# Kernel tuning notes

Measured on AMD Instinct MI355X. Metric: run time of the kernel, lower is better.

Reference implementation:

```python
import jax, jax.numpy as jnp
import numpy as np

C = 512
M = 8            # n_heads
G = 32           # GroupNorm groups
EPS = 1e-6


def setup_inputs() -> dict:
    key = jax.random.key(0)
    ks = jax.random.split(key, 7)
    x = jax.random.normal(ks[0], (2, C, 64, 64), dtype=jnp.float32)
    gn_weight = jnp.ones((C,), jnp.float32)
    gn_bias = jnp.zeros((C,), jnp.float32)
    qkv_w = jax.random.normal(ks[1], (3 * C, C), jnp.float32) * (1.0 / np.sqrt(C))
    qkv_b = jnp.zeros((3 * C,), jnp.float32)
    # source zero-inits proj_out; we use small random weights so the attention
    proj_w = jax.random.normal(ks[2], (C, C), jnp.float32) * (0.02 / np.sqrt(C))
    proj_b = jnp.zeros((C,), jnp.float32)
    return {"x": x, "gn_weight": gn_weight, "gn_bias": gn_bias,
            "qkv_w": qkv_w, "qkv_b": qkv_b, "proj_w": proj_w, "proj_b": proj_b}


def _forward(x, gn_weight, gn_bias, qkv_w, qkv_b, proj_w, proj_b):
    b, c, H, W = x.shape
    n = H * W
    d = c // M
    xf = x.reshape(b, c, n)

    # GroupNorm(32, c, eps=1e-6, affine)
    xg = xf.reshape(b, G, (c // G) * n)
    mu = xg.mean(axis=-1, keepdims=True)
    var = xg.var(axis=-1, keepdims=True)
    xn = ((xg - mu) * jax.lax.rsqrt(var + EPS)).reshape(b, c, n)
    xn = xn * gn_weight[None, :, None] + gn_bias[None, :, None]

    # 1x1 conv -> qkv, then legacy reshape-then-split
    qkv = jnp.einsum('oc,bcn->bon', qkv_w, xn) + qkv_b[None, :, None]  # (b, 3c, n)
    qkv = qkv.reshape(b * M, 3 * d, n)
    q, k, v = qkv[:, :d], qkv[:, d:2 * d], qkv[:, 2 * d:]

    scale = 1.0 / np.sqrt(np.sqrt(d))
    w = jnp.einsum('Bdi,Bdj->Bij', q * scale, k * scale)  # (b*m, n, n)
    w = jax.nn.softmax(w, axis=-1)
    a = jnp.einsum('Bin,Bdn->Bdi', w, v)                  # (b*m, d, n)
    a = a.reshape(b, c, n)

    h = jnp.einsum('oc,bcn->bon', proj_w, a) + proj_b[None, :, None]
    # NOTE: source reassigns x = norm(x) before the residual add.
    return (xn + h).reshape(b, c, H, W)


def reference(x, gn_weight, gn_bias, qkv_w, qkv_b, proj_w, proj_b):
    return _forward(x, gn_weight, gn_bias, qkv_w, qkv_b, proj_w, proj_b)
```

## Files before the change

kernel.cpp:

```cpp
#include <hip/hip_runtime.h>
#include <cstdint>
#include <cstddef>

typedef __attribute__((ext_vector_type(8))) short short8;
typedef __attribute__((ext_vector_type(4))) float f32x4;

#define QSCALE 0.18033688011112043f

__device__ __forceinline__ float bf2f(unsigned short u) {
  return __uint_as_float(((unsigned)u) << 16);
}
__device__ __forceinline__ unsigned short f2bf(float f) {
  unsigned u = __float_as_uint(f);
  u += 0x7fffu + ((u >> 16) & 1u);
  return (unsigned short)(u >> 16);
}
__device__ __forceinline__ unsigned packbf2(float a, float b) {
  unsigned ua = __float_as_uint(a) + 0x8000u;
  unsigned ub = __float_as_uint(b) + 0x8000u;
  return __builtin_amdgcn_perm(ub, ua, 0x07060302u);
}
__device__ __forceinline__ unsigned cvtpk(float a, float b) {
  unsigned r;
  asm("v_cvt_pk_bf16_f32 %0, %1, %2" : "=v"(r) : "v"(a), "v"(b));
  return r;
}
__device__ __forceinline__ short8 mk8(unsigned a, unsigned b, unsigned c, unsigned d) {
  union { unsigned u[4]; short8 s; } x;
  x.u[0] = a; x.u[1] = b; x.u[2] = c; x.u[3] = d;
  return x.s;
}
__device__ __forceinline__ void g2l16(const void* g, void* l) {
  __builtin_amdgcn_global_load_lds(
      (const __attribute__((address_space(1))) unsigned int*)g,
      (__attribute__((address_space(3))) unsigned int*)l, 16, 0, 0);
}

__global__ __launch_bounds__(256) void k_wconv(const float* __restrict__ wqf,
                                               const float* __restrict__ wpf,
                                               unsigned short* __restrict__ wq,
                                               unsigned short* __restrict__ wp) {
  int i = blockIdx.x * 256 + threadIdx.x;
  if (i < 196608) {
    float4 v = ((const float4*)wqf)[i];
    ushort4 u;
    u.x = f2bf(v.x); u.y = f2bf(v.y); u.z = f2bf(v.z); u.w = f2bf(v.w);
    ((ushort4*)wq)[i] = u;
  } else {
    int k = i - 196608;
    float4 v = ((const float4*)wpf)[k];
    ushort4 u;
    u.x = f2bf(v.x); u.y = f2bf(v.y); u.z = f2bf(v.z); u.w = f2bf(v.w);
    ((ushort4*)wp)[k] = u;
  }
}

__global__ __launch_bounds__(256) void k_gnpart(const float* __restrict__ x,
                                                float* __restrict__ part) {
  int blk = blockIdx.x;
  int bg = blk >> 4, slice = blk & 15;
  const float4* base = (const float4*)(x + (size_t)bg * 65536 + (size_t)slice * 4096);
  int t = threadIdx.x;
  float s = 0.f, q = 0.f;
#pragma unroll
  for (int i = 0; i < 4; ++i) {
    float4 v = base[t + i * 256];
    s += v.x + v.y + v.z + v.w;
    q += v.x * v.x + v.y * v.y + v.z * v.z + v.w * v.w;
  }
#pragma unroll
  for (int off = 1; off < 64; off <<= 1) {
    s += __shfl_xor(s, off);
    q += __shfl_xor(q, off);
  }
  __shared__ float red[8];
  int wid = t >> 6;
  if ((t & 63) == 0) { red[wid * 2] = s; red[wid * 2 + 1] = q; }
  __syncthreads();
  if (t == 0) {
    float S = red[0] + red[2] + red[4] + red[6];
    float Q = red[1] + red[3] + red[5] + red[7];
    part[blk * 2] = S;
    part[blk * 2 + 1] = Q;
  }
}

__global__ void k_gnfin(const float* __restrict__ part, float* __restrict__ stats) {
  int t = threadIdx.x;
  float S = 0.f, Q = 0.f;
#pragma unroll
  for (int i = 0; i < 16; ++i) {
    S += part[(t * 16 + i) * 2];
    Q += part[(t * 16 + i) * 2 + 1];
  }
  float mean = S * (1.f / 65536.f);
  float var = Q * (1.f / 65536.f) - mean * mean;
  stats[t * 2] = mean;
  stats[t * 2 + 1] = rsqrtf(var + 1e-6f);
}

__global__ __launch_bounds__(256) void k_gnnorm(const float* __restrict__ x,
                                                const float* __restrict__ gnw,
                                                const float* __restrict__ gnb,
                                                const float* __restrict__ stats,
                                                unsigned short* __restrict__ xn,
                                                unsigned short* __restrict__ xnT) {
  __shared__ float T[64 * 65];
  const int t = threadIdx.x;
  const int n0 = blockIdx.x * 64, c0 = blockIdx.y * 64, bb = blockIdx.z;
#pragma unroll
  for (int p = 0; p < 4; ++p) {
    int s = p * 256 + t;
    int row = s >> 4, seg = s & 15;
    int c = c0 + row;
    int gi = bb * 32 + (c >> 4);
    float mean = stats[gi * 2], rstd = stats[gi * 2 + 1];
    float gw = gnw[c] * rstd;
    float gb = gnb[c] - mean * gw;
    float4 v = *(const float4*)(x + ((size_t)bb * 512 + c) * 4096 + n0 + seg * 4);
    float f0 = v.x * gw + gb, f1 = v.y * gw + gb, f2 = v.z * gw + gb, f3 = v.w * gw + gb;
    ushort4 u;
    u.x = f2bf(f0); u.y = f2bf(f1); u.z = f2bf(f2); u.w = f2bf(f3);
    *(ushort4*)(xn + ((size_t)bb * 512 + c) * 4096 + n0 + seg * 4) = u;
    T[(seg * 4 + 0) * 65 + row] = f0;
    T[(seg * 4 + 1) * 65 + row] = f1;
    T[(seg * 4 + 2) * 65 + row] = f2;
    T[(seg * 4 + 3) * 65 + row] = f3;
  }
  __syncthreads();
#pragma unroll
  for (int p = 0; p < 4; ++p) {
    int s = p * 256 + t;
    int nl = s >> 4, cs = s & 15;
    float f0 = T[nl * 65 + cs * 4 + 0];
    float f1 = T[nl * 65 + cs * 4 + 1];
    float f2 = T[nl * 65 + cs * 4 + 2];
    float f3 = T[nl * 65 + cs * 4 + 3];
    ushort4 u;
    u.x = f2bf(f0); u.y = f2bf(f1); u.z = f2bf(f2); u.w = f2bf(f3);
    *(ushort4*)(xnT + ((size_t)bb * 4096 + n0 + nl) * 512 + c0 + cs * 4) = u;
  }
}

template <int MODE>
__global__ __launch_bounds__(256) void k_gemm(
    const unsigned short* __restrict__ A,
    const unsigned short* __restrict__ Bt,
    const float* __restrict__ bias,
    unsigned short* __restrict__ outA,
    unsigned short* __restrict__ outT,
    const unsigned short* __restrict__ resid,
    float* __restrict__ outF,
    int Mo) {
  __shared__ char lds[34816];
  const int t = threadIdx.x;
  const int lane = t & 63;
  const int g = lane >> 4, ln = lane & 15;
  const int wid = t >> 6, wr = wid >> 1, wc = wid & 1;
  const int bn0 = blockIdx.x * 128, bm0 = blockIdx.y * 128, bb = blockIdx.z;

  const unsigned short* Ab = A + (size_t)bm0 * 512;
  const unsigned short* Bb = Bt + ((size_t)bb * 4096 + bn0) * 512;

  f32x4 acc[4][4];
#pragma unroll
  for (int m = 0; m < 4; ++m)
#pragma unroll
    for (int n = 0; n < 4; ++n) acc[m][n] = f32x4{0.f, 0.f, 0.f, 0.f};

#pragma unroll 1
  for (int kt = 0; kt < 8; ++kt) {
#pragma unroll
    for (int p = 0; p < 4; ++p) {
      int s = p * 256 + t;
      int row = s >> 3;
      int csg = (s & 7) ^ (row & 7);
      g2l16(Ab + (size_t)row * 512 + kt * 64 + csg * 8,
            &lds[(p * 256 + (t & ~63)) * 16]);
    }
#pragma unroll
    for (int p = 0; p < 4; ++p) {
      int s = p * 256 + t;
      int row = s >> 3;
      int csg = (s & 7) ^ (row & 7);
      g2l16(Bb + (size_t)row * 512 + kt * 64 + csg * 8,
            &lds[16384 + (p * 256 + (t & ~63)) * 16]);
    }
    __syncthreads();
#pragma unroll
    for (int kk = 0; kk < 2; ++kk) {
      short8 af[4], bfr[4];
#pragma unroll
      for (int m = 0; m < 4; ++m) {
        int row = wr * 64 + m * 16 + ln;
        int cs = (kk * 4 + g) ^ (row & 7);
        af[m] = *(const short8*)&lds[row * 128 + cs * 16];
      }
#pragma unroll
      for (int n = 0; n < 4; ++n) {
        int row = wc * 64 + n * 16 + ln;
        int cs = (kk * 4 + g) ^ (row & 7);
        bfr[n] = *(const short8*)&lds[16384 + row * 128 + cs * 16];
      }
      __builtin_amdgcn_s_setprio(1);
#pragma unroll
      for (int m = 0; m < 4; ++m)
#pragma unroll
        for (int n = 0; n < 4; ++n)
          acc[m][n] = __builtin_amdgcn_mfma_f32_16x16x32_bf16(af[m], bfr[n], acc[m][n], 0, 0, 0);
      __builtin_amdgcn_s_setprio(0);
    }
    __syncthreads();
  }

  if (MODE == 0) {
#pragma unroll
    for (int m = 0; m < 4; ++m)
#pragma unroll
      for (int n = 0; n < 4; ++n)
#pragma unroll
        for (int r = 0; r < 4; ++r) {
          int ol = wr * 64 + m * 16 + g * 4 + r;
          int jl = wc * 64 + n * 16 + ln;
          int o = bm0 + ol, j = bn0 + jl;
          float v = acc[m][n][r] + bias[o];
          unsigned short bv = f2bf(v);
          if ((o % 192) >= 128) {
            int jp = (j & ~63) | (j & 32) | ((j & 0xC) << 1) | ((j & 16) >> 2) | (j & 3);
            outA[((size_t)bb * 1536 + o) * 4096 + jp] = bv;
          }
          *(unsigned short*)&lds[jl * 272 + ol * 2] = bv;
        }
    __syncthreads();
#pragma unroll
    for (int p = 0; p < 8; ++p) {
      int s = p * 256 + t;
      int jl = s >> 4, cs = s & 15;
      int oo = bm0 + cs * 8;
      if ((oo % 192) < 128) {
        short8 v = *(const short8*)&lds[jl * 272 + cs * 16];
        *(short8*)&outT[((size_t)bb * 4096 + bn0 + jl) * 1536 + oo] = v;
      }
    }
  } else {
#pragma unroll
    for (int m = 0; m < 4; ++m)
#pragma unroll
      for (int n = 0; n < 4; ++n)
#pragma unroll
        for (int r = 0; r < 4; ++r) {
          int o = bm0 + wr * 64 + m * 16 + g * 4 + r;
          int j = bn0 + wc * 64 + n * 16 + ln;
          size_t idx = ((size_t)bb * 512 + o) * 4096 + j;
          outF[idx] = acc[m][n][r] + bias[o] + bf2f(resid[idx]);
        }
  }
}

__global__ __launch_bounds__(256, 2) void k_attn(const unsigned short* __restrict__ qkv,
                                                 const unsigned short* __restrict__ qkvT,
                                                 unsigned short* __restrict__ aT) {
  __shared__ char lds[49152];
  const int t = threadIdx.x, lane = t & 63;
  const int g = lane >> 4, ln = lane & 15;
  const int wid = t >> 6;
  const int h = blockIdx.y, bb = blockIdx.z;
  const int q0 = blockIdx.x * 128 + wid * 32;

  int kaddr[2][4], vaddr[2][4];
#pragma unroll
  for (int kk = 0; kk < 2; ++kk)
#pragma unroll
    for (int f = 0; f < 4; ++f) {
      int row = f * 16 + ln;
      int off = row * 128 + (((kk * 4 + g) ^ (row & 7)) << 4);
      kaddr[kk][f] = off;
      vaddr[kk][f] = 24576 + off;
    }

  const unsigned short* kS[2];
  const unsigned short* vS[2];
  int ldst[2];
#pragma unroll
  for (int p = 0; p < 2; ++p) {
    int s = p * 256 + t;
    int row = s >> 3, csg = (s & 7) ^ (row & 7);
    kS[p] = qkvT + ((size_t)bb * 4096 + row) * 1536 + 192 * h + 64 + csg * 8;
    vS[p] = qkv + ((size_t)bb * 1536 + 192 * h + 128 + row) * 4096 + csg * 8;
    ldst[p] = (p * 256 + (t & ~63)) * 16;
  }

  short8 qf[2][2];
#pragma unroll
  for (int qt = 0; qt < 2; ++qt)
#pragma unroll
    for (int kk = 0; kk < 2; ++kk) {
      short8 v = *(const short8*)(qkvT + ((size_t)bb * 4096 + q0 + qt * 16 + ln) * 1536 +
                                  192 * h + kk * 32 + g * 8);
#pragma unroll
      for (int e = 0; e < 8; ++e) {
        float f = bf2f((unsigned short)v[e]) * QSCALE;
        v[e] = (short)f2bf(f);
      }
      qf[qt][kk] = v;
    }

  const short8 onesb = mk8(0x3F803F80u, 0x3F803F80u, 0x3F803F80u, 0x3F803F80u);

  f32x4 acc[2][4];
  f32x4 lacc[2];
#pragma unroll
  for (int qt = 0; qt < 2; ++qt) {
#pragma unroll
    for (int df = 0; df < 4; ++df) acc[qt][df] = f32x4{0.f, 0.f, 0.f, 0.f};
    lacc[qt] = f32x4{0.f, 0.f, 0.f, 0.f};
  }

#pragma unroll
  for (int jt = 0; jt < 2; ++jt) {
#pragma unroll
    for (int p = 0; p < 2; ++p) {
      g2l16(kS[p], &lds[jt * 8192 + ldst[p]]);
      g2l16(vS[p], &lds[24576 + jt * 8192 + ldst[p]]);
      kS[p] += 64 * 1536;
      vS[p] += 64;
    }
  }

#pragma unroll 3
  for (int jt = 0; jt < 64; ++jt) {
    const int cur = jt % 3;
    const char* Kc = &lds[cur * 8192];
    const char* Vc = &lds[cur * 8192];
    if (jt < 63) {
      asm volatile("s_waitcnt vmcnt(4)" ::: "memory");
    } else {
      asm volatile("s_waitcnt vmcnt(0)" ::: "memory");
    }
    __builtin_amdgcn_s_barrier();
    __builtin_amdgcn_sched_barrier(0);

    if (jt < 62) {
      int nb = (jt + 2) % 3;
#pragma unroll
      for (int p = 0; p < 2; ++p) {
        g2l16(kS[p], &lds[nb * 8192 + ldst[p]]);
        g2l16(vS[p], &lds[24576 + nb * 8192 + ldst[p]]);
        kS[p] += 64 * 1536;
        vS[p] += 64;
      }
    }

    short8 kf[2][4], vf[2][4];
#pragma unroll
    for (int kk = 0; kk < 2; ++kk)
#pragma unroll
      for (int f = 0; f < 4; ++f) {
        kf[kk][f] = *(const short8*)(Kc + kaddr[kk][f]);
        vf[kk][f] = *(const short8*)(Vc + vaddr[kk][f]);
      }

#pragma unroll
    for (int qt = 0; qt < 2; ++qt) {
      f32x4 w[4];
      const f32x4 zf = f32x4{0.f, 0.f, 0.f, 0.f};
      __builtin_amdgcn_s_setprio(1);
#pragma unroll
      for (int jf = 0; jf < 4; ++jf)
        w[jf] = __builtin_amdgcn_mfma_f32_16x16x32_bf16(kf[0][jf], qf[qt][0], zf, 0, 0, 0);
#pragma unroll
      for (int jf = 0; jf < 4; ++jf)
        w[jf] = __builtin_amdgcn_mfma_f32_16x16x32_bf16(kf[1][jf], qf[qt][1], w[jf], 0, 0, 0);
      __builtin_amdgcn_s_setprio(0);

#pragma unroll
      for (int jf = 0; jf < 4; ++jf)
#pragma unroll
        for (int r = 0; r < 4; ++r)
          w[jf][r] = __builtin_amdgcn_exp2f(w[jf][r]);

      short8 pf[2];
#pragma unroll
      for (int kk = 0; kk < 2; ++kk)
        pf[kk] = mk8(cvtpk(w[2 * kk][0], w[2 * kk][1]),
                     cvtpk(w[2 * kk][2], w[2 * kk][3]),
                     cvtpk(w[2 * kk + 1][0], w[2 * kk + 1][1]),
                     cvtpk(w[2 * kk + 1][2], w[2 * kk + 1][3]));

      __builtin_amdgcn_s_setprio(1);
#pragma unroll
      for (int kk = 0; kk < 2; ++kk) {
#pragma unroll
        for (int df = 0; df < 4; ++df)
          acc[qt][df] = __builtin_amdgcn_mfma_f32_16x16x32_bf16(pf[kk], vf[kk][df], acc[qt][df], 0, 0, 0);
        lacc[qt] = __builtin_amdgcn_mfma_f32_16x16x32_bf16(pf[kk], onesb, lacc[qt], 0, 0, 0);
      }
      __builtin_amdgcn_s_setprio(0);
    }
  }

#pragma unroll
  for (int qt = 0; qt < 2; ++qt) {
#pragma unroll
    for (int r = 0; r < 4; ++r) {
      float inv = 1.f / lacc[qt][r];
      int row = q0 + qt * 16 + g * 4 + r;
#pragma unroll
      for (int df = 0; df < 4; ++df)
        aT[((size_t)bb * 4096 + row) * 512 + h * 64 + df * 16 + ln] =
            f2bf(acc[qt][df][r] * inv);
    }
  }
}

extern "C" void kernel_launch(void* const* d_in, const int* in_sizes, int n_in,
                              void* d_out, int out_size, void* d_ws, size_t ws_size,
                              hipStream_t stream) {
  const float* x     = (const float*)d_in[0];
  const float* gnw   = (const float*)d_in[1];
  const float* gnb   = (const float*)d_in[2];
  const float* qkvw  = (const float*)d_in[3];
  const float* qkvb  = (const float*)d_in[4];
  const float* projw = (const float*)d_in[5];
  const float* projb = (const float*)d_in[6];
  float* out = (float*)d_out;
  char* ws = (char*)d_ws;

  const size_t OFF_WQ   = 0;
  const size_t OFF_WP   = 1572864;
  const size_t OFF_XN   = 2097152;
  const size_t OFF_XNT  = 10485760;
  const size_t OFF_QKV  = 18874368;
  const size_t OFF_QKVT = 44040192;
  const size_t OFF_AT   = 69206016;
  const size_t OFF_PART = 77594624;
  const size_t OFF_STAT = 77602816;

  unsigned short* wq   = (unsigned short*)(ws + OFF_WQ);
  unsigned short* wp   = (unsigned short*)(ws + OFF_WP);
  unsigned short* xn   = (unsigned short*)(ws + OFF_XN);
  unsigned short* xnT  = (unsigned short*)(ws + OFF_XNT);
  unsigned short* qkv  = (unsigned short*)(ws + OFF_QKV);
  unsigned short* qkvT = (unsigned short*)(ws + OFF_QKVT);
  unsigned short* aT   = (unsigned short*)(ws + OFF_AT);
  float* part  = (float*)(ws + OFF_PART);
  float* stats = (float*)(ws + OFF_STAT);

  k_wconv<<<dim3(1024), dim3(256), 0, stream>>>(qkvw, projw, wq, wp);
  k_gnpart<<<dim3(1024), dim3(256), 0, stream>>>(x, part);
  k_gnfin<<<dim3(1), dim3(64), 0, stream>>>(part, stats);
  k_gnnorm<<<dim3(64, 8, 2), dim3(256), 0, stream>>>(x, gnw, gnb, stats, xn, xnT);
  k_gemm<0><<<dim3(32, 12, 2), dim3(256), 0, stream>>>(wq, xnT, qkvb, qkv, qkvT, nullptr, nullptr, 1536);
  k_attn<<<dim3(32, 8, 2), dim3(256), 0, stream>>>(qkv, qkvT, aT);
  k_gemm<1><<<dim3(32, 4, 2), dim3(256), 0, stream>>>(wp, aT, projb, nullptr, nullptr, xn, out, 512);
}
```

Measured before the change: 131.4 us.

## Software-pipeline attention PV with next QK/exp and merge weight-convert with GN partials

The attention loop is restructured so that the PV MFMAs for the previous key tile run interleaved, via sched_group_barrier, with the QK MFMAs and exp2 work of the current tile. V fragments and P values are carried across iterations, with a prologue and epilogue for the first and last tiles. The aim is to hide exp/convert VALU latency behind matrix work. Separately, the weight-conversion and GroupNorm partial-sum kernels are merged into a single launch to save one kernel launch. The pipelining raises register pressure, and the interleave pattern may not match the real instruction mix.

Measured after the change: 125.6 us. 1.05x faster.

```diff
diff --git a/kernel.cpp b/kernel.cpp
--- a/kernel.cpp
+++ b/kernel.cpp
@@ -15,11 +15,6 @@
   u += 0x7fffu + ((u >> 16) & 1u);
   return (unsigned short)(u >> 16);
 }
-__device__ __forceinline__ unsigned packbf2(float a, float b) {
-  unsigned ua = __float_as_uint(a) + 0x8000u;
-  unsigned ub = __float_as_uint(b) + 0x8000u;
-  return __builtin_amdgcn_perm(ub, ua, 0x07060302u);
-}
 __device__ __forceinline__ unsigned cvtpk(float a, float b) {
   unsigned r;
   asm("v_cvt_pk_bf16_f32 %0, %1, %2" : "=v"(r) : "v"(a), "v"(b));
@@ -36,52 +31,54 @@
       (__attribute__((address_space(3))) unsigned int*)l, 16, 0, 0);
 }
 
-__global__ __launch_bounds__(256) void k_wconv(const float* __restrict__ wqf,
-                                               const float* __restrict__ wpf,
-                                               unsigned short* __restrict__ wq,
-                                               unsigned short* __restrict__ wp) {
-  int i = blockIdx.x * 256 + threadIdx.x;
-  if (i < 196608) {
-    float4 v = ((const float4*)wqf)[i];
-    ushort4 u;
-    u.x = f2bf(v.x); u.y = f2bf(v.y); u.z = f2bf(v.z); u.w = f2bf(v.w);
-    ((ushort4*)wq)[i] = u;
+__global__ __launch_bounds__(256) void k_wgn(const float* __restrict__ wqf,
+                                             const float* __restrict__ wpf,
+                                             unsigned short* __restrict__ wq,
+                                             unsigned short* __restrict__ wp,
+                                             const float* __restrict__ x,
+                                             float* __restrict__ part) {
+  __shared__ float red[8];
+  const int blk = blockIdx.x;
+  const int t = threadIdx.x;
+  if (blk < 1024) {
+    int i = blk * 256 + t;
+    if (i < 196608) {
+      float4 v = ((const float4*)wqf)[i];
+      ushort4 u;
+      u.x = f2bf(v.x); u.y = f2bf(v.y); u.z = f2bf(v.z); u.w = f2bf(v.w);
+      ((ushort4*)wq)[i] = u;
+    } else {
+      int k = i - 196608;
+      float4 v = ((const float4*)wpf)[k];
+      ushort4 u;
+      u.x = f2bf(v.x); u.y = f2bf(v.y); u.z = f2bf(v.z); u.w = f2bf(v.w);
+      ((ushort4*)wp)[k] = u;
+    }
   } else {
-    int k = i - 196608;
-    float4 v = ((const float4*)wpf)[k];
-    ushort4 u;
-    u.x = f2bf(v.x); u.y = f2bf(v.y); u.z = f2bf(v.z); u.w = f2bf(v.w);
-    ((ushort4*)wp)[k] = u;
-  }
-}
-
-__global__ __launch_bounds__(256) void k_gnpart(const float* __restrict__ x,
-                                                float* __restrict__ part) {
-  int blk = blockIdx.x;
-  int bg = blk >> 4, slice = blk & 15;
-  const float4* base = (const float4*)(x + (size_t)bg * 65536 + (size_t)slice * 4096);
-  int t = threadIdx.x;
-  float s = 0.f, q = 0.f;
-#pragma unroll
-  for (int i = 0; i < 4; ++i) {
-    float4 v = base[t + i * 256];
-    s += v.x + v.y + v.z + v.w;
-    q += v.x * v.x + v.y * v.y + v.z * v.z + v.w * v.w;
-  }
-#pragma unroll
-  for (int off = 1; off < 64; off <<= 1) {
-    s += __shfl_xor(s, off);
-    q += __shfl_xor(q, off);
-  }
-  __shared__ float red[8];
-  int wid = t >> 6;
-  if ((t & 63) == 0) { red[wid * 2] = s; red[wid * 2 + 1] = q; }
-  __syncthreads();
-  if (t == 0) {
-    float S = red[0] + red[2] + red[4] + red[6];
-    float Q = red[1] + red[3] + red[5] + red[7];
-    part[blk * 2] = S;
-    part[blk * 2 + 1] = Q;
+    int b2 = blk - 1024;
+    int bg = b2 >> 4, slice = b2 & 15;
+    const float4* base = (const float4*)(x + (size_t)bg * 65536 + (size_t)slice * 4096);
+    float s = 0.f, q = 0.f;
+#pragma unroll
+    for (int i = 0; i < 4; ++i) {
+      float4 v = base[t + i * 256];
+      s += v.x + v.y + v.z + v.w;
+      q += v.x * v.x + v.y * v.y + v.z * v.z + v.w * v.w;
+    }
+#pragma unroll
+    for (int off = 1; off < 64; off <<= 1) {
+      s += __shfl_xor(s, off);
+      q += __shfl_xor(q, off);
+    }
+    int wid = t >> 6;
+    if ((t & 63) == 0) { red[wid * 2] = s; red[wid * 2 + 1] = q; }
+    __syncthreads();
+    if (t == 0) {
+      float S = red[0] + red[2] + red[4] + red[6];
+      float Q = red[1] + red[3] + red[5] + red[7];
+      part[b2 * 2] = S;
+      part[b2 * 2 + 1] = Q;
+    }
   }
 }
 
@@ -316,6 +313,9 @@
     lacc[qt] = f32x4{0.f, 0.f, 0.f, 0.f};
   }
 
+  short8 pf[2][2];
+  short8 vfp[2][4];
+
 #pragma unroll
   for (int jt = 0; jt < 2; ++jt) {
 #pragma unroll
@@ -327,15 +327,71 @@
     }
   }
 
+  {
+    asm volatile("s_waitcnt vmcnt(4)" ::: "memory");
+    __builtin_amdgcn_s_barrier();
+    __builtin_amdgcn_sched_barrier(0);
+#pragma unroll
+    for (int p = 0; p < 2; ++p) {
+      g2l16(kS[p], &lds[2 * 8192 + ldst[p]]);
+      g2l16(vS[p], &lds[24576 + 2 * 8192 + ldst[p]]);
+      kS[p] += 64 * 1536;
+      vS[p] += 64;
+    }
+    const char* Kc = &lds[0];
+    short8 kf[2][4];
+#pragma unroll
+    for (int kk = 0; kk < 2; ++kk)
+#pragma unroll
+      for (int f = 0; f < 4; ++f) kf[kk][f] = *(const short8*)(Kc + kaddr[kk][f]);
+    const f32x4 zf = f32x4{0.f, 0.f, 0.f, 0.f};
+    f32x4 w0[4], w1[4];
+    __builtin_amdgcn_s_setprio(1);
+#pragma unroll
+    for (int jf = 0; jf < 4; ++jf)
+      w0[jf] = __builtin_amdgcn_mfma_f32_16x16x32_bf16(kf[0][jf], qf[0][0], zf, 0, 0, 0);
+#pragma unroll
+    for (int jf = 0; jf < 4; ++jf)
+      w0[jf] = __builtin_amdgcn_mfma_f32_16x16x32_bf16(kf[1][jf], qf[0][1], w0[jf], 0, 0, 0);
+#pragma unroll
+    for (int jf = 0; jf < 4; ++jf)
+      w1[jf] = __builtin_amdgcn_mfma_f32_16x16x32_bf16(kf[0][jf], qf[1][0], zf, 0, 0, 0);
+#pragma unroll
+    for (int jf = 0; jf < 4; ++jf)
+      w1[jf] = __builtin_amdgcn_mfma_f32_16x16x32_bf16(kf[1][jf], qf[1][1], w1[jf], 0, 0, 0);
+    __builtin_amdgcn_s_setprio(0);
+#pragma unroll
+    for (int jf = 0; jf < 4; ++jf)
+#pragma unroll
+      for (int r = 0; r < 4; ++r) {
+        w0[jf][r] = __builtin_amdgcn_exp2f(w0[jf][r]);
+        w1[jf][r] = __builtin_amdgcn_exp2f(w1[jf][r]);
+      }
+#pragma unroll
+    for (int kk = 0; kk < 2; ++kk) {
+      pf[0][kk] = mk8(cvtpk(w0[2 * kk][0], w0[2 * kk][1]),
+                      cvtpk(w0[2 * kk][2], w0[2 * kk][3]),
+                      cvtpk(w0[2 * kk + 1][0], w0[2 * kk + 1][1]),
+                      cvtpk(w0[2 * kk + 1][2], w0[2 * kk + 1][3]));
+      pf[1][kk] = mk8(cvtpk(w1[2 * kk][0], w1[2 * kk][1]),
+                      cvtpk(w1[2 * kk][2], w1[2 * kk][3]),
+                      cvtpk(w1[2 * kk + 1][0], w1[2 * kk + 1][1]),
+                      cvtpk(w1[2 * kk + 1][2], w1[2 * kk + 1][3]));
+    }
+#pragma unroll
+    for (int kk = 0; kk < 2; ++kk)
+#pragma unroll
+      for (int f = 0; f < 4; ++f) vfp[kk][f] = *(const short8*)(Kc + vaddr[kk][f]);
+  }
+
 #pragma unroll 3
-  for (int jt = 0; jt < 64; ++jt) {
+  for (int jt = 1; jt < 64; ++jt) {
     const int cur = jt % 3;
     const char* Kc = &lds[cur * 8192];
-    const char* Vc = &lds[cur * 8192];
     if (jt < 63) {
-      asm volatile("s_waitcnt vmcnt(4)" ::: "memory");
+      asm volatile("s_waitcnt vmcnt(4) lgkmcnt(0)" ::: "memory");
     } else {
-      asm volatile("s_waitcnt vmcnt(0)" ::: "memory");
+      asm volatile("s_waitcnt vmcnt(0) lgkmcnt(0)" ::: "memory");
     }
     __builtin_amdgcn_s_barrier();
     __builtin_amdgcn_sched_barrier(0);
@@ -351,53 +407,86 @@
       }
     }
 
-    short8 kf[2][4], vf[2][4];
+    short8 kf[2][4];
 #pragma unroll
     for (int kk = 0; kk < 2; ++kk)
 #pragma unroll
-      for (int f = 0; f < 4; ++f) {
-        kf[kk][f] = *(const short8*)(Kc + kaddr[kk][f]);
-        vf[kk][f] = *(const short8*)(Vc + vaddr[kk][f]);
-      }
-
-#pragma unroll
-    for (int qt = 0; qt < 2; ++qt) {
-      f32x4 w[4];
-      const f32x4 zf = f32x4{0.f, 0.f, 0.f, 0.f};
-      __builtin_amdgcn_s_setprio(1);
-#pragma unroll
-      for (int jf = 0; jf < 4; ++jf)
-        w[jf] = __builtin_amdgcn_mfma_f32_16x16x32_bf16(kf[0][jf], qf[qt][0], zf, 0, 0, 0);
-#pragma unroll
-      for (int jf = 0; jf < 4; ++jf)
-        w[jf] = __builtin_amdgcn_mfma_f32_16x16x32_bf16(kf[1][jf], qf[qt][1], w[jf], 0, 0, 0);
-      __builtin_amdgcn_s_setprio(0);
-
-#pragma unroll
-      for (int jf = 0; jf < 4; ++jf)
-#pragma unroll
-        for (int r = 0; r < 4; ++r)
-          w[jf][r] = __builtin_amdgcn_exp2f(w[jf][r]);
-
-      short8 pf[2];
-#pragma unroll
-      for (int kk = 0; kk < 2; ++kk)
-        pf[kk] = mk8(cvtpk(w[2 * kk][0], w[2 * kk][1]),
-                     cvtpk(w[2 * kk][2], w[2 * kk][3]),
-                     cvtpk(w[2 * kk + 1][0], w[2 * kk + 1][1]),
-                     cvtpk(w[2 * kk + 1][2], w[2 * kk + 1][3]));
-
-      __builtin_amdgcn_s_setprio(1);
+      for (int f = 0; f < 4; ++f) kf[kk][f] = *(const short8*)(Kc + kaddr[kk][f]);
+
+    const f32x4 zf = f32x4{0.f, 0.f, 0.f, 0.f};
+    f32x4 w0[4], w1[4];
+    __builtin_amdgcn_s_setprio(1);
+#pragma unroll
+    for (int jf = 0; jf < 4; ++jf)
+      w0[jf] = __builtin_amdgcn_mfma_f32_16x16x32_bf16(kf[0][jf], qf[0][0], zf, 0, 0, 0);
+#pragma unroll
+    for (int jf = 0; jf < 4; ++jf)
+      w0[jf] = __builtin_amdgcn_mfma_f32_16x16x32_bf16(kf[1][jf], qf[0][1], w0[jf], 0, 0, 0);
+#pragma unroll
+    for (int jf = 0; jf < 4; ++jf)
+      w1[jf] = __builtin_amdgcn_mfma_f32_16x16x32_bf16(kf[0][jf], qf[1][0], zf, 0, 0, 0);
+#pragma unroll
+    for (int jf = 0; jf < 4; ++jf)
+      w1[jf] = __builtin_amdgcn_mfma_f32_16x16x32_bf16(kf[1][jf], qf[1][1], w1[jf], 0, 0, 0);
+    __builtin_amdgcn_sched_barrier(0);
+
+#pragma unroll
+    for (int jf = 0; jf < 4; ++jf)
+#pragma unroll
+      for (int r = 0; r < 4; ++r) {
+        w0[jf][r] = __builtin_amdgcn_exp2f(w0[jf][r]);
+        w1[jf][r] = __builtin_amdgcn_exp2f(w1[jf][r]);
+      }
+    short8 npf0[2], npf1[2];
+#pragma unroll
+    for (int kk = 0; kk < 2; ++kk) {
+      npf0[kk] = mk8(cvtpk(w0[2 * kk][0], w0[2 * kk][1]),
+                     cvtpk(w0[2 * kk][2], w0[2 * kk][3]),
+                     cvtpk(w0[2 * kk + 1][0], w0[2 * kk + 1][1]),
+                     cvtpk(w0[2 * kk + 1][2], w0[2 * kk + 1][3]));
+      npf1[kk] = mk8(cvtpk(w1[2 * kk][0], w1[2 * kk][1]),
+                     cvtpk(w1[2 * kk][2], w1[2 * kk][3]),
+                     cvtpk(w1[2 * kk + 1][0], w1[2 * kk + 1][1]),
+                     cvtpk(w1[2 * kk + 1][2], w1[2 * kk + 1][3]));
+    }
+#pragma unroll
+    for (int qt = 0; qt < 2; ++qt)
 #pragma unroll
       for (int kk = 0; kk < 2; ++kk) {
 #pragma unroll
         for (int df = 0; df < 4; ++df)
-          acc[qt][df] = __builtin_amdgcn_mfma_f32_16x16x32_bf16(pf[kk], vf[kk][df], acc[qt][df], 0, 0, 0);
-        lacc[qt] = __builtin_amdgcn_mfma_f32_16x16x32_bf16(pf[kk], onesb, lacc[qt], 0, 0, 0);
-      }
-      __builtin_amdgcn_s_setprio(0);
-    }
-  }
+          acc[qt][df] = __builtin_amdgcn_mfma_f32_16x16x32_bf16(pf[qt][kk], vfp[kk][df],
+                                                                acc[qt][df], 0, 0, 0);
+        lacc[qt] = __builtin_amdgcn_mfma_f32_16x16x32_bf16(pf[qt][kk], onesb, lacc[qt], 0, 0, 0);
+      }
+#pragma unroll
+    for (int i = 0; i < 20; ++i) {
+      __builtin_amdgcn_sched_group_barrier(0x8, 1, 0);
+      __builtin_amdgcn_sched_group_barrier(0x2, 2, 0);
+    }
+    __builtin_amdgcn_sched_barrier(0);
+    __builtin_amdgcn_s_setprio(0);
+
+    pf[0][0] = npf0[0]; pf[0][1] = npf0[1];
+    pf[1][0] = npf1[0]; pf[1][1] = npf1[1];
+#pragma unroll
+    for (int kk = 0; kk < 2; ++kk)
+#pragma unroll
+      for (int f = 0; f < 4; ++f) vfp[kk][f] = *(const short8*)(Kc + vaddr[kk][f]);
+  }
+
+  __builtin_amdgcn_s_setprio(1);
+#pragma unroll
+  for (int qt = 0; qt < 2; ++qt)
+#pragma unroll
+    for (int kk = 0; kk < 2; ++kk) {
+#pragma unroll
+      for (int df = 0; df < 4; ++df)
+        acc[qt][df] = __builtin_amdgcn_mfma_f32_16x16x32_bf16(pf[qt][kk], vfp[kk][df],
+                                                              acc[qt][df], 0, 0, 0);
+      lacc[qt] = __builtin_amdgcn_mfma_f32_16x16x32_bf16(pf[qt][kk], onesb, lacc[qt], 0, 0, 0);
+    }
+  __builtin_amdgcn_s_setprio(0);
 
 #pragma unroll
   for (int qt = 0; qt < 2; ++qt) {
@@ -446,8 +535,7 @@
   float* part  = (float*)(ws + OFF_PART);
   float* stats = (float*)(ws + OFF_STAT);
 
-  k_wconv<<<dim3(1024), dim3(256), 0, stream>>>(qkvw, projw, wq, wp);
-  k_gnpart<<<dim3(1024), dim3(256), 0, stream>>>(x, part);
+  k_wgn<<<dim3(2048), dim3(256), 0, stream>>>(qkvw, projw, wq, wp, x, part);
   k_gnfin<<<dim3(1), dim3(64), 0, stream>>>(part, stats);
   k_gnnorm<<<dim3(64, 8, 2), dim3(256), 0, stream>>>(x, gnw, gnb, stats, xn, xnT);
   k_gemm<0><<<dim3(32, 12, 2), dim3(256), 0, stream>>>(wq, xnT, qkvb, qkv, qkvT, nullptr, nullptr, 1536);
```

## Software-pipeline attention PV with 8 waves per block, fuse weight-convert and GN-partial kernels

Applied to the files above, without the earlier changes.

The attention kernel moves to 512 threads per block, with each wave owning 16 query rows instead of 32. The loop is software-pipelined so the PV MFMAs for the previous tile overlap the QK MFMAs and exp of the current tile, and sched_group_barrier interleaves MFMA with LDS reads. Separately, the weight bf16 conversion and the GroupNorm partial-sum kernels are merged into one launch to save launch overhead. The risks are register pressure under launch_bounds(512,4) and more barrier contention with 8 waves sharing each LDS tile.

Result: no change. 130.4 us (-0.8%).

```diff
diff --git a/kernel.cpp b/kernel.cpp
--- a/kernel.cpp
+++ b/kernel.cpp
@@ -15,11 +15,6 @@
   u += 0x7fffu + ((u >> 16) & 1u);
   return (unsigned short)(u >> 16);
 }
-__device__ __forceinline__ unsigned packbf2(float a, float b) {
-  unsigned ua = __float_as_uint(a) + 0x8000u;
-  unsigned ub = __float_as_uint(b) + 0x8000u;
-  return __builtin_amdgcn_perm(ub, ua, 0x07060302u);
-}
 __device__ __forceinline__ unsigned cvtpk(float a, float b) {
   unsigned r;
   asm("v_cvt_pk_bf16_f32 %0, %1, %2" : "=v"(r) : "v"(a), "v"(b));
@@ -36,52 +31,54 @@
       (__attribute__((address_space(3))) unsigned int*)l, 16, 0, 0);
 }
 
-__global__ __launch_bounds__(256) void k_wconv(const float* __restrict__ wqf,
-                                               const float* __restrict__ wpf,
-                                               unsigned short* __restrict__ wq,
-                                               unsigned short* __restrict__ wp) {
-  int i = blockIdx.x * 256 + threadIdx.x;
-  if (i < 196608) {
-    float4 v = ((const float4*)wqf)[i];
-    ushort4 u;
-    u.x = f2bf(v.x); u.y = f2bf(v.y); u.z = f2bf(v.z); u.w = f2bf(v.w);
-    ((ushort4*)wq)[i] = u;
+__global__ __launch_bounds__(256) void k_wgn(const float* __restrict__ wqf,
+                                             const float* __restrict__ wpf,
+                                             unsigned short* __restrict__ wq,
+                                             unsigned short* __restrict__ wp,
+                                             const float* __restrict__ x,
+                                             float* __restrict__ part) {
+  __shared__ float red[8];
+  const int blk = blockIdx.x;
+  const int t = threadIdx.x;
+  if (blk < 1024) {
+    int i = blk * 256 + t;
+    if (i < 196608) {
+      float4 v = ((const float4*)wqf)[i];
+      ushort4 u;
+      u.x = f2bf(v.x); u.y = f2bf(v.y); u.z = f2bf(v.z); u.w = f2bf(v.w);
+      ((ushort4*)wq)[i] = u;
+    } else {
+      int k = i - 196608;
+      float4 v = ((const float4*)wpf)[k];
+      ushort4 u;
+      u.x = f2bf(v.x); u.y = f2bf(v.y); u.z = f2bf(v.z); u.w = f2bf(v.w);
+      ((ushort4*)wp)[k] = u;
+    }
   } else {
-    int k = i - 196608;
-    float4 v = ((const float4*)wpf)[k];
-    ushort4 u;
-    u.x = f2bf(v.x); u.y = f2bf(v.y); u.z = f2bf(v.z); u.w = f2bf(v.w);
-    ((ushort4*)wp)[k] = u;
-  }
-}
-
-__global__ __launch_bounds__(256) void k_gnpart(const float* __restrict__ x,
-                                                float* __restrict__ part) {
-  int blk = blockIdx.x;
-  int bg = blk >> 4, slice = blk & 15;
-  const float4* base = (const float4*)(x + (size_t)bg * 65536 + (size_t)slice * 4096);
-  int t = threadIdx.x;
-  float s = 0.f, q = 0.f;
-#pragma unroll
-  for (int i = 0; i < 4; ++i) {
-    float4 v = base[t + i * 256];
-    s += v.x + v.y + v.z + v.w;
-    q += v.x * v.x + v.y * v.y + v.z * v.z + v.w * v.w;
-  }
-#pragma unroll
-  for (int off = 1; off < 64; off <<= 1) {
-    s += __shfl_xor(s, off);
-    q += __shfl_xor(q, off);
-  }
-  __shared__ float red[8];
-  int wid = t >> 6;
-  if ((t & 63) == 0) { red[wid * 2] = s; red[wid * 2 + 1] = q; }
-  __syncthreads();
-  if (t == 0) {
-    float S = red[0] + red[2] + red[4] + red[6];
-    float Q = red[1] + red[3] + red[5] + red[7];
-    part[blk * 2] = S;
-    part[blk * 2 + 1] = Q;
+    int b2 = blk - 1024;
+    int bg = b2 >> 4, slice = b2 & 15;
+    const float4* base = (const float4*)(x + (size_t)bg * 65536 + (size_t)slice * 4096);
+    float s = 0.f, q = 0.f;
+#pragma unroll
+    for (int i = 0; i < 4; ++i) {
+      float4 v = base[t + i * 256];
+      s += v.x + v.y + v.z + v.w;
+      q += v.x * v.x + v.y * v.y + v.z * v.z + v.w * v.w;
+    }
+#pragma unroll
+    for (int off = 1; off < 64; off <<= 1) {
+      s += __shfl_xor(s, off);
+      q += __shfl_xor(q, off);
+    }
+    int wid = t >> 6;
+    if ((t & 63) == 0) { red[wid * 2] = s; red[wid * 2 + 1] = q; }
+    __syncthreads();
+    if (t == 0) {
+      float S = red[0] + red[2] + red[4] + red[6];
+      float Q = red[1] + red[3] + red[5] + red[7];
+      part[b2 * 2] = S;
+      part[b2 * 2 + 1] = Q;
+    }
   }
 }
 
@@ -257,7 +254,7 @@
   }
 }
 
-__global__ __launch_bounds__(256, 2) void k_attn(const unsigned short* __restrict__ qkv,
+__global__ __launch_bounds__(512, 4) void k_attn(const unsigned short* __restrict__ qkv,
                                                  const unsigned short* __restrict__ qkvT,
                                                  unsigned short* __restrict__ aT) {
   __shared__ char lds[49152];
@@ -265,7 +262,7 @@
   const int g = lane >> 4, ln = lane & 15;
   const int wid = t >> 6;
   const int h = blockIdx.y, bb = blockIdx.z;
-  const int q0 = blockIdx.x * 128 + wid * 32;
+  const int q0 = blockIdx.x * 128 + wid * 16;
 
   int kaddr[2][4], vaddr[2][4];
 #pragma unroll
@@ -278,138 +275,176 @@
       vaddr[kk][f] = 24576 + off;
     }
 
-  const unsigned short* kS[2];
-  const unsigned short* vS[2];
-  int ldst[2];
-#pragma unroll
-  for (int p = 0; p < 2; ++p) {
-    int s = p * 256 + t;
-    int row = s >> 3, csg = (s & 7) ^ (row & 7);
-    kS[p] = qkvT + ((size_t)bb * 4096 + row) * 1536 + 192 * h + 64 + csg * 8;
-    vS[p] = qkv + ((size_t)bb * 1536 + 192 * h + 128 + row) * 4096 + csg * 8;
-    ldst[p] = (p * 256 + (t & ~63)) * 16;
-  }
-
-  short8 qf[2][2];
-#pragma unroll
-  for (int qt = 0; qt < 2; ++qt)
-#pragma unroll
-    for (int kk = 0; kk < 2; ++kk) {
-      short8 v = *(const short8*)(qkvT + ((size_t)bb * 4096 + q0 + qt * 16 + ln) * 1536 +
-                                  192 * h + kk * 32 + g * 8);
-#pragma unroll
-      for (int e = 0; e < 8; ++e) {
-        float f = bf2f((unsigned short)v[e]) * QSCALE;
-        v[e] = (short)f2bf(f);
-      }
-      qf[qt][kk] = v;
-    }
+  const unsigned short* kS;
+  const unsigned short* vS;
+  int ldst;
+  {
+    int row = t >> 3, csg = (t & 7) ^ (row & 7);
+    kS = qkvT + ((size_t)bb * 4096 + row) * 1536 + 192 * h + 64 + csg * 8;
+    vS = qkv + ((size_t)bb * 1536 + 192 * h + 128 + row) * 4096 + csg * 8;
+    ldst = (t & ~63) * 16;
+  }
+
+  short8 qf[2];
+#pragma unroll
+  for (int kk = 0; kk < 2; ++kk) {
+    short8 v = *(const short8*)(qkvT + ((size_t)bb * 4096 + q0 + ln) * 1536 +
+                                192 * h + kk * 32 + g * 8);
+#pragma unroll
+    for (int e = 0; e < 8; ++e) {
+      float f = bf2f((unsigned short)v[e]) * QSCALE;
+      v[e] = (short)f2bf(f);
+    }
+    qf[kk] = v;
+  }
 
   const short8 onesb = mk8(0x3F803F80u, 0x3F803F80u, 0x3F803F80u, 0x3F803F80u);
 
-  f32x4 acc[2][4];
-  f32x4 lacc[2];
-#pragma unroll
-  for (int qt = 0; qt < 2; ++qt) {
-#pragma unroll
-    for (int df = 0; df < 4; ++df) acc[qt][df] = f32x4{0.f, 0.f, 0.f, 0.f};
-    lacc[qt] = f32x4{0.f, 0.f, 0.f, 0.f};
-  }
+  f32x4 acc[4];
+  f32x4 lacc = f32x4{0.f, 0.f, 0.f, 0.f};
+#pragma unroll
+  for (int df = 0; df < 4; ++df) acc[df] = f32x4{0.f, 0.f, 0.f, 0.f};
+
+  short8 pf[2];
+  short8 vfp[2][4];
 
 #pragma unroll
   for (int jt = 0; jt < 2; ++jt) {
-#pragma unroll
-    for (int p = 0; p < 2; ++p) {
-      g2l16(kS[p], &lds[jt * 8192 + ldst[p]]);
-      g2l16(vS[p], &lds[24576 + jt * 8192 + ldst[p]]);
-      kS[p] += 64 * 1536;
-      vS[p] += 64;
-    }
+    g2l16(kS, &lds[jt * 8192 + ldst]);
+    g2l16(vS, &lds[24576 + jt * 8192 + ldst]);
+    kS += 64 * 1536;
+    vS += 64;
+  }
+
+  {
+    asm volatile("s_waitcnt vmcnt(2)" ::: "memory");
+    __builtin_amdgcn_s_barrier();
+    __builtin_amdgcn_sched_barrier(0);
+    g2l16(kS, &lds[2 * 8192 + ldst]);
+    g2l16(vS, &lds[24576 + 2 * 8192 + ldst]);
+    kS += 64 * 1536;
+    vS += 64;
+    const char* Kc = &lds[0];
+    short8 kf[2][4];
+#pragma unroll
+    for (int kk = 0; kk < 2; ++kk)
+#pragma unroll
+      for (int f = 0; f < 4; ++f) kf[kk][f] = *(const short8*)(Kc + kaddr[kk][f]);
+    const f32x4 zf = f32x4{0.f, 0.f, 0.f, 0.f};
+    f32x4 w[4];
+    __builtin_amdgcn_s_setprio(1);
+#pragma unroll
+    for (int jf = 0; jf < 4; ++jf)
+      w[jf] = __builtin_amdgcn_mfma_f32_16x16x32_bf16(kf[0][jf], qf[0], zf, 0, 0, 0);
+#pragma unroll
+    for (int jf = 0; jf < 4; ++jf)
+      w[jf] = __builtin_amdgcn_mfma_f32_16x16x32_bf16(kf[1][jf], qf[1], w[jf], 0, 0, 0);
+    __builtin_amdgcn_s_setprio(0);
+#pragma unroll
+    for (int jf = 0; jf < 4; ++jf)
+#pragma unroll
+      for (int r = 0; r < 4; ++r) w[jf][r] = __builtin_amdgcn_exp2f(w[jf][r]);
+#pragma unroll
+    for (int kk = 0; kk < 2; ++kk)
+      pf[kk] = mk8(cvtpk(w[2 * kk][0], w[2 * kk][1]),
+                   cvtpk(w[2 * kk][2], w[2 * kk][3]),
+                   cvtpk(w[2 * kk + 1][0], w[2 * kk + 1][1]),
+                   cvtpk(w[2 * kk + 1][2], w[2 * kk + 1][3]));
+#pragma unroll
+    for (int kk = 0; kk < 2; ++kk)
+#pragma unroll
+      for (int f = 0; f < 4; ++f) vfp[kk][f] = *(const short8*)(Kc + vaddr[kk][f]);
   }
 
 #pragma unroll 3
-  for (int jt = 0; jt < 64; ++jt) {
+  for (int jt = 1; jt < 64; ++jt) {
     const int cur = jt % 3;
     const char* Kc = &lds[cur * 8192];
-    const char* Vc = &lds[cur * 8192];
     if (jt < 63) {
-      asm volatile("s_waitcnt vmcnt(4)" ::: "memory");
+      asm volatile("s_waitcnt vmcnt(2) lgkmcnt(0)" ::: "memory");
     } else {
-      asm volatile("s_waitcnt vmcnt(0)" ::: "memory");
+      asm volatile("s_waitcnt vmcnt(0) lgkmcnt(0)" ::: "memory");
     }
     __builtin_amdgcn_s_barrier();
     __builtin_amdgcn_sched_barrier(0);
 
     if (jt < 62) {
       int nb = (jt + 2) % 3;
-#pragma unroll
-      for (int p = 0; p < 2; ++p) {
-        g2l16(kS[p], &lds[nb * 8192 + ldst[p]]);
-        g2l16(vS[p], &lds[24576 + nb * 8192 + ldst[p]]);
-        kS[p] += 64 * 1536;
-        vS[p] += 64;
-      }
-    }
-
-    short8 kf[2][4], vf[2][4];
-#pragma unroll
-    for (int kk = 0; kk < 2; ++kk)
-#pragma unroll
-      for (int f = 0; f < 4; ++f) {
-        kf[kk][f] = *(const short8*)(Kc + kaddr[kk][f]);
-        vf[kk][f] = *(const short8*)(Vc + vaddr[kk][f]);
-      }
-
-#pragma unroll
-    for (int qt = 0; qt < 2; ++qt) {
-      f32x4 w[4];
-      const f32x4 zf = f32x4{0.f, 0.f, 0.f, 0.f};
-      __builtin_amdgcn_s_setprio(1);
-#pragma unroll
-      for (int jf = 0; jf < 4; ++jf)
-        w[jf] = __builtin_amdgcn_mfma_f32_16x16x32_bf16(kf[0][jf], qf[qt][0], zf, 0, 0, 0);
-#pragma unroll
-      for (int jf = 0; jf < 4; ++jf)
-        w[jf] = __builtin_amdgcn_mfma_f32_16x16x32_bf16(kf[1][jf], qf[qt][1], w[jf], 0, 0, 0);
-      __builtin_amdgcn_s_setprio(0);
-
-#pragma unroll
-      for (int jf = 0; jf < 4; ++jf)
-#pragma unroll
-        for (int r = 0; r < 4; ++r)
-          w[jf][r] = __builtin_amdgcn_exp2f(w[jf][r]);
-
-      short8 pf[2];
-#pragma unroll
-      for (int kk = 0; kk < 2; ++kk)
-        pf[kk] = mk8(cvtpk(w[2 * kk][0], w[2 * kk][1]),
-                     cvtpk(w[2 * kk][2], w[2 * kk][3]),
-                     cvtpk(w[2 * kk + 1][0], w[2 * kk + 1][1]),
-                     cvtpk(w[2 * kk + 1][2], w[2 * kk + 1][3]));
-
-      __builtin_amdgcn_s_setprio(1);
-#pragma unroll
-      for (int kk = 0; kk < 2; ++kk) {
-#pragma unroll
-        for (int df = 0; df < 4; ++df)
-          acc[qt][df] = __builtin_amdgcn_mfma_f32_16x16x32_bf16(pf[kk], vf[kk][df], acc[qt][df], 0, 0, 0);
-        lacc[qt] = __builtin_amdgcn_mfma_f32_16x16x32_bf16(pf[kk], onesb, lacc[qt], 0, 0, 0);
-      }
-      __builtin_amdgcn_s_setprio(0);
-    }
-  }
-
-#pragma unroll
-  for (int qt = 0; qt < 2; ++qt) {
-#pragma unroll
-    for (int r = 0; r < 4; ++r) {
-      float inv = 1.f / lacc[qt][r];
-      int row = q0 + qt * 16 + g * 4 + r;
+      g2l16(kS, &lds[nb * 8192 + ldst]);
+      g2l16(vS, &lds[24576 + nb * 8192 + ldst]);
+      kS += 64 * 1536;
+      vS += 64;
+    }
+
+    short8 kf[2][4];
+#pragma unroll
+    for (int kk = 0; kk < 2; ++kk)
+#pragma unroll
+      for (int f = 0; f < 4; ++f) kf[kk][f] = *(const short8*)(Kc + kaddr[kk][f]);
+
+    const f32x4 zf = f32x4{0.f, 0.f, 0.f, 0.f};
+    f32x4 w[4];
+    __builtin_amdgcn_s_setprio(1);
+#pragma unroll
+    for (int jf = 0; jf < 4; ++jf)
+      w[jf] = __builtin_amdgcn_mfma_f32_16x16x32_bf16(kf[0][jf], qf[0], zf, 0, 0, 0);
+#pragma unroll
+    for (int jf = 0; jf < 4; ++jf)
+      w[jf] = __builtin_amdgcn_mfma_f32_16x16x32_bf16(kf[1][jf], qf[1], w[jf], 0, 0, 0);
+    __builtin_amdgcn_sched_barrier(0);
+
+#pragma unroll
+    for (int jf = 0; jf < 4; ++jf)
+#pragma unroll
+      for (int r = 0; r < 4; ++r) w[jf][r] = __builtin_amdgcn_exp2f(w[jf][r]);
+    short8 npf[2];
+#pragma unroll
+    for (int kk = 0; kk < 2; ++kk)
+      npf[kk] = mk8(cvtpk(w[2 * kk][0], w[2 * kk][1]),
+                    cvtpk(w[2 * kk][2], w[2 * kk][3]),
+                    cvtpk(w[2 * kk + 1][0], w[2 * kk + 1][1]),
+                    cvtpk(w[2 * kk + 1][2], w[2 * kk + 1][3]));
+#pragma unroll
+    for (int kk = 0; kk < 2; ++kk) {
 #pragma unroll
       for (int df = 0; df < 4; ++df)
-        aT[((size_t)bb * 4096 + row) * 512 + h * 64 + df * 16 + ln] =
-            f2bf(acc[qt][df][r] * inv);
-    }
+        acc[df] = __builtin_amdgcn_mfma_f32_16x16x32_bf16(pf[kk], vfp[kk][df], acc[df], 0, 0, 0);
+      lacc = __builtin_amdgcn_mfma_f32_16x16x32_bf16(pf[kk], onesb, lacc, 0, 0, 0);
+    }
+#pragma unroll
+    for (int i = 0; i < 10; ++i) {
+      __builtin_amdgcn_sched_group_barrier(0x8, 1, 0);
+      __builtin_amdgcn_sched_group_barrier(0x2, 2, 0);
+    }
+    __builtin_amdgcn_sched_barrier(0);
+    __builtin_amdgcn_s_setprio(0);
+
+    pf[0] = npf[0];
+    pf[1] = npf[1];
+#pragma unroll
+    for (int kk = 0; kk < 2; ++kk)
+#pragma unroll
+      for (int f = 0; f < 4; ++f) vfp[kk][f] = *(const short8*)(Kc + vaddr[kk][f]);
+  }
+
+  __builtin_amdgcn_s_setprio(1);
+#pragma unroll
+  for (int kk = 0; kk < 2; ++kk) {
+#pragma unroll
+    for (int df = 0; df < 4; ++df)
+      acc[df] = __builtin_amdgcn_mfma_f32_16x16x32_bf16(pf[kk], vfp[kk][df], acc[df], 0, 0, 0);
+    lacc = __builtin_amdgcn_mfma_f32_16x16x32_bf16(pf[kk], onesb, lacc, 0, 0, 0);
+  }
+  __builtin_amdgcn_s_setprio(0);
+
+#pragma unroll
+  for (int r = 0; r < 4; ++r) {
+    float inv = 1.f / lacc[r];
+    int row = q0 + g * 4 + r;
+#pragma unroll
+    for (int df = 0; df < 4; ++df)
+      aT[((size_t)bb * 4096 + row) * 512 + h * 64 + df * 16 + ln] =
+          f2bf(acc[df][r] * inv);
   }
 }
 
@@ -446,11 +481,10 @@
   float* part  = (float*)(ws + OFF_PART);
   float* stats = (float*)(ws + OFF_STAT);
 
-  k_wconv<<<dim3(1024), dim3(256), 0, stream>>>(qkvw, projw, wq, wp);
-  k_gnpart<<<dim3(1024), dim3(256), 0, stream>>>(x, part);
+  k_wgn<<<dim3(2048), dim3(256), 0, stream>>>(qkvw, projw, wq, wp, x, part);
   k_gnfin<<<dim3(1), dim3(64), 0, stream>>>(part, stats);
   k_gnnorm<<<dim3(64, 8, 2), dim3(256), 0, stream>>>(x, gnw, gnb, stats, xn, xnT);
   k_gemm<0><<<dim3(32, 12, 2), dim3(256), 0, stream>>>(wq, xnT, qkvb, qkv, qkvT, nullptr, nullptr, 1536);
-  k_attn<<<dim3(32, 8, 2), dim3(256), 0, stream>>>(qkv, qkvT, aT);
+  k_attn<<<dim3(32, 8, 2), dim3(512), 0, stream>>>(qkv, qkvT, aT);
   k_gemm<1><<<dim3(32, 4, 2), dim3(256), 0, stream>>>(wp, aT, projb, nullptr, nullptr, xn, out, 512);
 }
```
